# Performance work log

Measured on AMD Instinct MI355X. Metric: run time of the kernel, lower is better.

## Reference

```python
import jax, jax.numpy as jnp
import numpy as np

N_ATOMS = 500000
N_EDGES = 16000000
MAX_Z = 94


def setup_inputs() -> dict:
    key = jax.random.key(0)
    k1, k2, k3, k4 = jax.random.split(key, 4)
    Z = jax.random.randint(k1, (N_ATOMS,), 0, MAX_Z, dtype=jnp.int32)
    # distances in a physically plausible short range (ZBL is a short-range repulsion)
    Dij = jax.random.uniform(k2, (N_EDGES,), dtype=jnp.float32)
    idx_i = jnp.sort(jax.random.randint(k3, (N_EDGES,), 0, N_ATOMS, dtype=jnp.int32))
    idx_j = jax.random.randint(k4, (N_EDGES,), 0, N_ATOMS, dtype=jnp.int32)
    # learned parameters (defaults from ZBL.__init__)
    p = jnp.float32(0.23)
    d = jnp.float32(0.885)
    c = jnp.array([0.1818, 0.5099, 0.2802, 0.02817], dtype=jnp.float32)
    a = jnp.array([3.2, 0.9423, 0.4028, 0.2016], dtype=jnp.float32)
    return {"Z": Z, "Dij": Dij, "idx_i": idx_i, "idx_j": idx_j,
            "p": p, "d": d, "c": c, "a": a}


def reference(Z, Dij, idx_i, idx_j, p, d, c, a):
    # gather per-edge atomic numbers
    Zi = Z[idx_i].astype(Dij.dtype)  # [E]
    Zj = Z[idx_j].astype(Dij.dtype)  # [E]
    # NOTE: the original computes pre = Zi*Zj/Dij but never uses it in vij;
    # we reproduce the math actually returned.
    expv = Dij / d * (Zi ** p + Zj ** p)  # [E]
    # sum over the 4 screening terms: c[k] * exp(-a[k] * expv)
    vij = jnp.einsum("k,ke->e", c, jnp.exp(-a[:, None] * expv[None, :]))  # [E]
    # per-atom reduction (tf.math.segment_sum with sorted idx_i)
    return jax.ops.segment_sum(vij, idx_i, num_segments=N_ATOMS)  # [N]
```

## Files before the change

### kernel.cpp

```cpp
#include <hip/hip_runtime.h>


#define EPT   16
#define BLOCK 256
#define MAXZ  95

__device__ __forceinline__ float fast_exp2(float x) {
#if __has_builtin(__builtin_amdgcn_exp2f)
    return __builtin_amdgcn_exp2f(x);
#else
    return exp2f(x);
#endif
}

__global__ void __launch_bounds__(BLOCK) zbl_stage_kernel(
    const int* __restrict__ Z, const float* __restrict__ p,
    unsigned char* __restrict__ z8, float* __restrict__ zpf,
    float* __restrict__ ptab, int n)
{
    int i = blockIdx.x * BLOCK + threadIdx.x;
    if (i < MAXZ) ptab[i] = powf((float)i, p[0]);
    if (i < n) {
        int z = Z[i];
        z8[i]  = (unsigned char)z;
        zpf[i] = powf((float)z, p[0]);
    }
}

__global__ void __launch_bounds__(BLOCK) zbl_edge_kernel(
    const float*         __restrict__ Dij,
    const int*           __restrict__ idx_i,
    const int*           __restrict__ idx_j,
    const unsigned char* __restrict__ z8,
    const float*         __restrict__ zpf,
    const float*         __restrict__ ptab_g,
    const float*         __restrict__ dptr,
    const float*         __restrict__ c,
    const float*         __restrict__ a,
    float*               __restrict__ out,
    long long E)
{
    __shared__ float pt[MAXZ + 1];
    for (int k = threadIdx.x; k < MAXZ; k += BLOCK) pt[k] = ptab_g[k];
    __syncthreads();

    const long long t    = (long long)blockIdx.x * BLOCK + threadIdx.x;
    const long long base = t * EPT;
    if (base >= E) return;

    const float LOG2E = 1.4426950408889634f;
    const float invd  = 1.0f / dptr[0];
    const float m0 = -a[0] * LOG2E * invd;
    const float m1 = -a[1] * LOG2E * invd;
    const float m2 = -a[2] * LOG2E * invd;
    const float m3 = -a[3] * LOG2E * invd;
    const float c0 = c[0], c1 = c[1], c2 = c[2], c3 = c[3];

    if (base + EPT <= E) {
        float dv[EPT];
        int   iv[EPT], jv[EPT];
#pragma unroll
        for (int v = 0; v < EPT; v += 4) {
            const float4 dq = *reinterpret_cast<const float4*>(Dij  + base + v);
            const int4   iq = *reinterpret_cast<const int4*>(idx_i + base + v);
            const int4   jq = *reinterpret_cast<const int4*>(idx_j + base + v);
            dv[v] = dq.x; dv[v+1] = dq.y; dv[v+2] = dq.z; dv[v+3] = dq.w;
            iv[v] = iq.x; iv[v+1] = iq.y; iv[v+2] = iq.z; iv[v+3] = iq.w;
            jv[v] = jq.x; jv[v+1] = jq.y; jv[v+2] = jq.z; jv[v+3] = jq.w;
        }
        float zpj[EPT];
#pragma unroll
        for (int k = 0; k < EPT; ++k) {
            zpj[k] = __hip_atomic_load(zpf + jv[k], __ATOMIC_RELAXED,
                                       __HIP_MEMORY_SCOPE_AGENT);
        }
        int zi[EPT];
#pragma unroll
        for (int k = 0; k < EPT; ++k) zi[k] = z8[iv[k]];

        int   cur = iv[0];
        float acc = 0.0f;
#pragma unroll
        for (int k = 0; k < EPT; ++k) {
            const float tt = dv[k] * (pt[zi[k]] + zpj[k]);
            float v;
            v = c0 * fast_exp2(m0 * tt);
            v = fmaf(c1, fast_exp2(m1 * tt), v);
            v = fmaf(c2, fast_exp2(m2 * tt), v);
            v = fmaf(c3, fast_exp2(m3 * tt), v);
            if (iv[k] != cur) { atomicAdd(out + cur, acc); acc = 0.0f; cur = iv[k]; }
            acc += v;
        }
        atomicAdd(out + cur, acc);
    } else {
        int   cur = idx_i[base];
        float acc = 0.0f;
        for (long long e = base; e < E; ++e) {
            const int   i  = idx_i[e];
            const float zj = __hip_atomic_load(zpf + idx_j[e], __ATOMIC_RELAXED,
                                               __HIP_MEMORY_SCOPE_AGENT);
            const float tt = Dij[e] * (pt[z8[i]] + zj);
            float v;
            v = c0 * fast_exp2(m0 * tt);
            v = fmaf(c1, fast_exp2(m1 * tt), v);
            v = fmaf(c2, fast_exp2(m2 * tt), v);
            v = fmaf(c3, fast_exp2(m3 * tt), v);
            if (i != cur) { atomicAdd(out + cur, acc); acc = 0.0f; cur = i; }
            acc += v;
        }
        atomicAdd(out + cur, acc);
    }
}

extern "C" void kernel_launch(void* const* d_in, const int* in_sizes, int n_in,
                              void* d_out, int out_size, void* d_ws, size_t ws_size,
                              hipStream_t stream)
{
    const int*   Z     = (const int*)  d_in[0];
    const float* Dij   = (const float*)d_in[1];
    const int*   idx_i = (const int*)  d_in[2];
    const int*   idx_j = (const int*)  d_in[3];
    const float* p     = (const float*)d_in[4];
    const float* d     = (const float*)d_in[5];
    const float* c     = (const float*)d_in[6];
    const float* a     = (const float*)d_in[7];
    float*       out   = (float*)d_out;

    const int       nAtoms = in_sizes[0];
    const long long E      = in_sizes[1];

    float*         zpf  = (float*)d_ws;
    unsigned char* z8   = (unsigned char*)d_ws + (size_t)nAtoms * sizeof(float);
    size_t         poff = ((size_t)nAtoms * sizeof(float) + (size_t)nAtoms + 63) & ~(size_t)63;
    float*         ptab = (float*)((char*)d_ws + poff);

    (void)hipMemsetAsync(d_out, 0, (size_t)out_size * sizeof(float), stream);

    zbl_stage_kernel<<<(nAtoms + BLOCK - 1) / BLOCK, BLOCK, 0, stream>>>(
        Z, p, z8, zpf, ptab, nAtoms);

    const long long nThreads = (E + EPT - 1) / EPT;
    const int       nBlocks  = (int)((nThreads + BLOCK - 1) / BLOCK);
    zbl_edge_kernel<<<nBlocks, BLOCK, 0, stream>>>(
        Dij, idx_i, idx_j, z8, zpf, ptab, d, c, a, out, E);
}
```

Measured before the change: 256.7 us.

## Drop staging kernel, compute pow table per block, wave-reduce segment atomics

Removes the separate per-atom staging kernel. Each block now computes the 95-entry Z^p table in shared memory, and the Z values for both endpoints are gathered directly from the int32 Z array. After the per-thread run accumulation, a wave-level segmented scan over lanes combines partial sums that share the same atom key, so that only one atomicAdd is issued per key per wavefront. This trades the staging launch and the byte-sized z8 gather for 4-byte Z gathers, a powf per block, and the shuffle-scan overhead.

```diff
diff --git a/kernel.cpp b/kernel.cpp
--- a/kernel.cpp
+++ b/kernel.cpp
@@ -13,35 +13,20 @@
 #endif
 }
 
-__global__ void __launch_bounds__(BLOCK) zbl_stage_kernel(
-    const int* __restrict__ Z, const float* __restrict__ p,
-    unsigned char* __restrict__ z8, float* __restrict__ zpf,
-    float* __restrict__ ptab, int n)
-{
-    int i = blockIdx.x * BLOCK + threadIdx.x;
-    if (i < MAXZ) ptab[i] = powf((float)i, p[0]);
-    if (i < n) {
-        int z = Z[i];
-        z8[i]  = (unsigned char)z;
-        zpf[i] = powf((float)z, p[0]);
-    }
-}
-
 __global__ void __launch_bounds__(BLOCK) zbl_edge_kernel(
-    const float*         __restrict__ Dij,
-    const int*           __restrict__ idx_i,
-    const int*           __restrict__ idx_j,
-    const unsigned char* __restrict__ z8,
-    const float*         __restrict__ zpf,
-    const float*         __restrict__ ptab_g,
-    const float*         __restrict__ dptr,
-    const float*         __restrict__ c,
-    const float*         __restrict__ a,
-    float*               __restrict__ out,
+    const float* __restrict__ Dij,
+    const int*   __restrict__ idx_i,
+    const int*   __restrict__ idx_j,
+    const int*   __restrict__ Z,
+    const float* __restrict__ pptr,
+    const float* __restrict__ dptr,
+    const float* __restrict__ c,
+    const float* __restrict__ a,
+    float*       __restrict__ out,
     long long E)
 {
-    __shared__ float pt[MAXZ + 1];
-    for (int k = threadIdx.x; k < MAXZ; k += BLOCK) pt[k] = ptab_g[k];
+    __shared__ float pt[MAXZ];
+    if (threadIdx.x < MAXZ) pt[threadIdx.x] = powf((float)threadIdx.x, pptr[0]);
     __syncthreads();
 
     const long long t    = (long long)blockIdx.x * BLOCK + threadIdx.x;
@@ -56,6 +41,9 @@
     const float m3 = -a[3] * LOG2E * invd;
     const float c0 = c[0], c1 = c[1], c2 = c[2], c3 = c[3];
 
+    const long long waveBase = (t & ~63LL) * EPT;
+    const bool waveFull = (waveBase + 64LL * EPT) <= E;
+
     if (base + EPT <= E) {
         float dv[EPT];
         int   iv[EPT], jv[EPT];
@@ -68,21 +56,25 @@
             iv[v] = iq.x; iv[v+1] = iq.y; iv[v+2] = iq.z; iv[v+3] = iq.w;
             jv[v] = jq.x; jv[v+1] = jq.y; jv[v+2] = jq.z; jv[v+3] = jq.w;
         }
-        float zpj[EPT];
+        int zj[EPT];
 #pragma unroll
         for (int k = 0; k < EPT; ++k) {
-            zpj[k] = __hip_atomic_load(zpf + jv[k], __ATOMIC_RELAXED,
-                                       __HIP_MEMORY_SCOPE_AGENT);
+            zj[k] = __hip_atomic_load(Z + jv[k], __ATOMIC_RELAXED,
+                                      __HIP_MEMORY_SCOPE_AGENT);
         }
         int zi[EPT];
 #pragma unroll
-        for (int k = 0; k < EPT; ++k) zi[k] = z8[iv[k]];
+        for (int k = 0; k < EPT; ++k) zi[k] = Z[iv[k]];
+
+        float zz[EPT];
+#pragma unroll
+        for (int k = 0; k < EPT; ++k) zz[k] = pt[zi[k]] + pt[zj[k]];
 
         int   cur = iv[0];
         float acc = 0.0f;
 #pragma unroll
         for (int k = 0; k < EPT; ++k) {
-            const float tt = dv[k] * (pt[zi[k]] + zpj[k]);
+            const float tt = dv[k] * zz[k];
             float v;
             v = c0 * fast_exp2(m0 * tt);
             v = fmaf(c1, fast_exp2(m1 * tt), v);
@@ -91,15 +83,30 @@
             if (iv[k] != cur) { atomicAdd(out + cur, acc); acc = 0.0f; cur = iv[k]; }
             acc += v;
         }
-        atomicAdd(out + cur, acc);
+
+        if (waveFull) {
+            const int lane = threadIdx.x & 63;
+            float vv  = acc;
+            int   key = cur;
+#pragma unroll
+            for (int d2 = 1; d2 < 64; d2 <<= 1) {
+                const float u  = __shfl_up(vv, d2, 64);
+                const int   pk = __shfl_up(key, d2, 64);
+                if (lane >= d2 && pk == key) vv += u;
+            }
+            const int nk = __shfl_down(key, 1, 64);
+            if (lane == 63 || nk != key) atomicAdd(out + key, vv);
+        } else {
+            atomicAdd(out + cur, acc);
+        }
     } else {
         int   cur = idx_i[base];
         float acc = 0.0f;
         for (long long e = base; e < E; ++e) {
-            const int   i  = idx_i[e];
-            const float zj = __hip_atomic_load(zpf + idx_j[e], __ATOMIC_RELAXED,
-                                               __HIP_MEMORY_SCOPE_AGENT);
-            const float tt = Dij[e] * (pt[z8[i]] + zj);
+            const int i  = idx_i[e];
+            const int zj = __hip_atomic_load(Z + idx_j[e], __ATOMIC_RELAXED,
+                                             __HIP_MEMORY_SCOPE_AGENT);
+            const float tt = Dij[e] * (pt[Z[i]] + pt[zj]);
             float v;
             v = c0 * fast_exp2(m0 * tt);
             v = fmaf(c1, fast_exp2(m1 * tt), v);
@@ -126,21 +133,12 @@
     const float* a     = (const float*)d_in[7];
     float*       out   = (float*)d_out;
 
-    const int       nAtoms = in_sizes[0];
-    const long long E      = in_sizes[1];
-
-    float*         zpf  = (float*)d_ws;
-    unsigned char* z8   = (unsigned char*)d_ws + (size_t)nAtoms * sizeof(float);
-    size_t         poff = ((size_t)nAtoms * sizeof(float) + (size_t)nAtoms + 63) & ~(size_t)63;
-    float*         ptab = (float*)((char*)d_ws + poff);
+    const long long E = in_sizes[1];
 
     (void)hipMemsetAsync(d_out, 0, (size_t)out_size * sizeof(float), stream);
-
-    zbl_stage_kernel<<<(nAtoms + BLOCK - 1) / BLOCK, BLOCK, 0, stream>>>(
-        Z, p, z8, zpf, ptab, nAtoms);
 
     const long long nThreads = (E + EPT - 1) / EPT;
     const int       nBlocks  = (int)((nThreads + BLOCK - 1) / BLOCK);
     zbl_edge_kernel<<<nBlocks, BLOCK, 0, stream>>>(
-        Dij, idx_i, idx_j, z8, zpf, ptab, d, c, a, out, E);
+        Dij, idx_i, idx_j, Z, p, d, c, a, out, E);
 }
```

Measured after the change: 248.8 us. -3.1%, faster.
